# Kernel optimization log

Measured on AMD Instinct MI355X. Metric: run time of the kernel, lower is better.

The kernel has to match this reference:

```python
import jax, jax.numpy as jnp
import numpy as np

B, H, S, D = 2, 12, 2048, 64


def setup_inputs() -> dict:
    key = jax.random.key(0)
    kq, kk, kv = jax.random.split(key, 3)
    q = jax.random.normal(kq, (B, H, S, D), dtype=jnp.float32)
    k = jax.random.normal(kk, (B, H, S, D), dtype=jnp.float32)
    v = jax.random.normal(kv, (B, H, S, D), dtype=jnp.float32)
    # causal mask: True = attend (keep), lower triangle
    mask = jnp.tril(jnp.ones((S, S), dtype=bool))
    return {"q": q, "k": k, "v": v, "mask": mask}


def reference(q, k, v, mask):
    dim = q.shape[-1]
    # [B,H,S,S] scores
    scores = jnp.einsum("bhqd,bhkd->bhqk", q, k) / jnp.sqrt(jnp.asarray(dim, q.dtype))
    # dynamic mask-direction logic from the original module:
    # if the mask is denser in the strict upper triangle, True means "mask out";
    # otherwise True means "keep".
    sq = mask.shape[-1]
    sample = mask.reshape(-1, sq, sq)[0]
    upper = jnp.triu(jnp.ones_like(sample, dtype=bool), k=1)
    flip = jnp.sum(sample & upper) > jnp.sum(sample & ~upper)
    keep = jnp.where(flip, ~mask, mask)  # True = keep
    neg_inf = jnp.asarray(-jnp.inf, scores.dtype)
    scores = jnp.where(keep, scores, neg_inf)
    weights = jax.nn.softmax(scores, axis=-1)
    # dropout with p_drop=0.0 is the identity
    return jnp.einsum("bhqk,bhkd->bhqd", weights, v)
```

## Files before the change

kernel.cpp:

```cpp
#include <hip/hip_runtime.h>
#include <hip/hip_bf16.h>


#define SEQ 2048
#define DH 64
#define NHEADS 24
#define BN 64
#define LDK 72
#define ELEMS_PER_TENSOR (NHEADS * SEQ * DH)
#define NSLOT5 (NHEADS * 16 * 4)
#define WS_BF16  ((size_t)3 * ELEMS_PER_TENSOR * 2)
#define WS_FA7   (WS_BF16 + (size_t)NSLOT5 * 8192 * 2 + (size_t)NSLOT5 * 128 * 4)

typedef float f32x4 __attribute__((ext_vector_type(4)));
typedef __bf16 bf16x8 __attribute__((ext_vector_type(8)));
typedef __bf16 bf16x4 __attribute__((ext_vector_type(4)));

#if __has_builtin(__builtin_amdgcn_exp2f)
#define EXP2F(x) __builtin_amdgcn_exp2f(x)
#else
#define EXP2F(x) exp2f(x)
#endif

#define QSCALE 0.1803368801111204f

__global__ __launch_bounds__(256)
void prep_kernel(const float* __restrict__ q, const float* __restrict__ k,
                 const float* __restrict__ v,
                 __bf16* __restrict__ qs, __bf16* __restrict__ ks,
                 __bf16* __restrict__ vt)
{
    __shared__ __bf16 T[64][LDK];
    const int bx = blockIdx.x;
    const int tid = threadIdx.x;
    if (bx < 3072) {
        const int t = bx * 256 + tid;
        const int half = ELEMS_PER_TENSOR / 8;
        const bool is_q = t < half;
        const int idx = (is_q ? t : t - half) * 8;
        const float* src = is_q ? q : k;
        const float sc = is_q ? QSCALE : 1.0f;
        f32x4 a = *(const f32x4*)(src + idx);
        f32x4 b = *(const f32x4*)(src + idx + 4);
        bf16x8 o;
        #pragma unroll
        for (int j = 0; j < 4; ++j) { o[j] = (__bf16)(a[j] * sc); o[4 + j] = (__bf16)(b[j] * sc); }
        *(bf16x8*)((is_q ? qs : ks) + idx) = o;
    } else {
        const int b2 = bx - 3072;
        const int bh = b2 >> 5;
        const int s0 = (b2 & 31) * 64;
        const int r = tid >> 2, c0 = (tid & 3) * 16;
        const float* vp = v + (size_t)bh * SEQ * DH + (size_t)(s0 + r) * DH + c0;
        __bf16 tmp[16];
        #pragma unroll
        for (int jj = 0; jj < 16; ++jj) tmp[jj] = (__bf16)vp[jj];
        *(bf16x8*)&T[r][c0]     = *(bf16x8*)&tmp[0];
        *(bf16x8*)&T[r][c0 + 8] = *(bf16x8*)&tmp[8];
        __syncthreads();
        const int d = tid >> 2, j0 = (tid & 3) * 16;
        __bf16 o[16];
        #pragma unroll
        for (int jj = 0; jj < 16; ++jj) o[jj] = T[j0 + jj][d];
        __bf16* op = vt + (size_t)bh * DH * SEQ + (size_t)d * SEQ + s0 + j0;
        *(bf16x8*)op       = *(bf16x8*)&o[0];
        *(bf16x8*)(op + 8) = *(bf16x8*)&o[8];
    }
}

__global__ __launch_bounds__(256, 3)
void fa7_kernel(const __bf16* __restrict__ qs, const __bf16* __restrict__ ks,
                const __bf16* __restrict__ vt,
                __bf16* __restrict__ opart, float* __restrict__ lpart)
{
    const int bx = blockIdx.x;
    const int xcd = bx & 7;
    const int sub = bx >> 3;
    const int bh = (sub / 40) * 8 + xcd;
    const int rem = 39 - (sub % 40);
    int mt2, st;
    if      (rem >= 36) { mt2 = 15; st = 36; }
    else if (rem >= 32) { mt2 = 14; st = 32; }
    else if (rem >= 28) { mt2 = 13; st = 28; }
    else if (rem >= 24) { mt2 = 12; st = 24; }
    else if (rem >= 21) { mt2 = 11; st = 21; }
    else if (rem >= 18) { mt2 = 10; st = 18; }
    else if (rem >= 15) { mt2 = 9;  st = 15; }
    else if (rem >= 12) { mt2 = 8;  st = 12; }
    else if (rem >= 10) { mt2 = 7;  st = 10; }
    else if (rem >= 8)  { mt2 = 6;  st = 8; }
    else if (rem >= 6)  { mt2 = 5;  st = 6; }
    else if (rem >= 4)  { mt2 = 4;  st = 4; }
    else                { mt2 = rem; st = rem; }
    const int chunk = rem - st;
    const int jt0 = chunk * 8;
    const int jt_end = min(jt0 + 8, 2 * mt2 + 2);
    const int q0 = mt2 * 128;

    const int tid = threadIdx.x;
    const int w = tid >> 6, lane = tid & 63;
    const int g = lane >> 4, li = lane & 15;

    __shared__ __bf16 Ks[2][64 * 64];
    __shared__ __bf16 Vs[2][64 * 64];
    __shared__ __bf16 Ps[4 * 32 * 64];

    const __bf16* qh = qs + (size_t)bh * SEQ * DH;
    const __bf16* kh = ks + (size_t)bh * SEQ * DH;
    const __bf16* vh = vt + (size_t)bh * DH * SEQ;

    bf16x8 qf[2][2];
    #pragma unroll
    for (int a = 0; a < 2; ++a) {
        const __bf16* qp = qh + (size_t)(q0 + w * 32 + a * 16 + li) * DH + g * 8;
        qf[a][0] = *(const bf16x8*)qp;
        qf[a][1] = *(const bf16x8*)(qp + 32);
    }

    bf16x8 ones;
    #pragma unroll
    for (int j = 0; j < 8; ++j) ones[j] = (__bf16)1.0f;

    f32x4 acc[2][4] = {};
    f32x4 accl[2] = {};

    const int srow0 = tid >> 3;
    const int sg    = tid & 7;

    bf16x8 kr[2], vr[2];
    #pragma unroll
    for (int s = 0; s < 2; ++s) {
        const int row = s * 32 + srow0;
        const int lg = sg ^ (row & 7);
        kr[s] = *(const bf16x8*)(kh + (size_t)(jt0 * BN + row) * DH + lg * 8);
        vr[s] = *(const bf16x8*)(vh + (size_t)row * SEQ + jt0 * BN + lg * 8);
    }
    #pragma unroll
    for (int s = 0; s < 2; ++s) {
        *(bf16x8*)((char*)Ks[0] + s * 4096 + tid * 16) = kr[s];
        *(bf16x8*)((char*)Vs[0] + s * 4096 + tid * 16) = vr[s];
    }
    if (jt0 + 1 < jt_end) {
        const int kv1 = (jt0 + 1) * BN;
        #pragma unroll
        for (int s = 0; s < 2; ++s) {
            const int row = s * 32 + srow0;
            const int lg = sg ^ (row & 7);
            kr[s] = *(const bf16x8*)(kh + (size_t)(kv1 + row) * DH + lg * 8);
            vr[s] = *(const bf16x8*)(vh + (size_t)row * SEQ + kv1 + lg * 8);
        }
    }
    __syncthreads();

    int buf = 0;
    for (int jt = jt0; jt < jt_end; ++jt) {
        if (jt + 1 < jt_end) {
            #pragma unroll
            for (int s = 0; s < 2; ++s) {
                *(bf16x8*)((char*)Ks[buf ^ 1] + s * 4096 + tid * 16) = kr[s];
                *(bf16x8*)((char*)Vs[buf ^ 1] + s * 4096 + tid * 16) = vr[s];
            }
        }
        if (jt + 2 < jt_end) {
            const int kv2 = (jt + 2) * BN;
            #pragma unroll
            for (int s = 0; s < 2; ++s) {
                const int row = s * 32 + srow0;
                const int lg = sg ^ (row & 7);
                kr[s] = *(const bf16x8*)(kh + (size_t)(kv2 + row) * DH + lg * 8);
                vr[s] = *(const bf16x8*)(vh + (size_t)row * SEQ + kv2 + lg * 8);
            }
        }

        const char* Kb = (const char*)Ks[buf];
        const char* Vb = (const char*)Vs[buf];
        float s4[2][4][4];
        #pragma unroll
        for (int t = 0; t < 4; ++t) {
            f32x4 sa0 = {}, sa1 = {};
            #pragma unroll
            for (int c = 0; c < 2; ++c) {
                bf16x8 kf = *(const bf16x8*)(Kb +
                    (t * 16 + li) * 128 + (((c * 4 + g) ^ (li & 7)) << 4));
                sa0 = __builtin_amdgcn_mfma_f32_16x16x32_bf16(kf, qf[0][c], sa0, 0, 0, 0);
                sa1 = __builtin_amdgcn_mfma_f32_16x16x32_bf16(kf, qf[1][c], sa1, 0, 0, 0);
            }
            #pragma unroll
            for (int r = 0; r < 4; ++r) { s4[0][t][r] = sa0[r]; s4[1][t][r] = sa1[r]; }
        }

        if (jt >= 2 * mt2) {
            #pragma unroll
            for (int a = 0; a < 2; ++a) {
                const int qr = q0 + w * 32 + a * 16 + li;
                #pragma unroll
                for (int t = 0; t < 4; ++t) {
                    #pragma unroll
                    for (int r = 0; r < 4; ++r)
                        if (jt * 64 + t * 16 + g * 4 + r > qr) s4[a][t][r] = -1e30f;
                }
            }
        }

        #pragma unroll
        for (int a = 0; a < 2; ++a) {
            const int row = a * 16 + li;
            #pragma unroll
            for (int t = 0; t < 4; ++t) {
                bf16x4 p4;
                #pragma unroll
                for (int r = 0; r < 4; ++r) p4[r] = (__bf16)EXP2F(s4[a][t][r]);
                const int pg = (t * 2 + (g >> 1)) ^ (li & 7);
                *(bf16x4*)((char*)Ps + w * 4096 + row * 128 + (pg << 4) + ((g & 1) << 3)) = p4;
            }
        }

        #pragma unroll
        for (int c = 0; c < 2; ++c) {
            const int pgp = ((c * 4 + g) ^ (li & 7)) << 4;
            bf16x8 pf0 = *(const bf16x8*)((const char*)Ps + w * 4096 + li * 128 + pgp);
            bf16x8 pf1 = *(const bf16x8*)((const char*)Ps + w * 4096 + (16 + li) * 128 + pgp);
            accl[0] = __builtin_amdgcn_mfma_f32_16x16x32_bf16(pf0, ones, accl[0], 0, 0, 0);
            accl[1] = __builtin_amdgcn_mfma_f32_16x16x32_bf16(pf1, ones, accl[1], 0, 0, 0);
            #pragma unroll
            for (int t = 0; t < 4; ++t) {
                bf16x8 vf = *(const bf16x8*)(Vb + (t * 16 + li) * 128 + pgp);
                acc[0][t] = __builtin_amdgcn_mfma_f32_16x16x32_bf16(pf0, vf, acc[0][t], 0, 0, 0);
                acc[1][t] = __builtin_amdgcn_mfma_f32_16x16x32_bf16(pf1, vf, acc[1][t], 0, 0, 0);
            }
        }

        if (jt + 1 < jt_end) __syncthreads();
        buf ^= 1;
    }

    const int slot = (bh * 16 + mt2) * 4 + chunk;
    __bf16* po = opart + (size_t)slot * 8192;
    #pragma unroll
    for (int a = 0; a < 2; ++a) {
        #pragma unroll
        for (int r = 0; r < 4; ++r) {
            const int row = w * 32 + a * 16 + g * 4 + r;
            __bf16* op = po + row * 64 + li;
            #pragma unroll
            for (int t = 0; t < 4; ++t) op[t * 16] = (__bf16)acc[a][t][r];
            if (li == 0) lpart[(size_t)slot * 128 + row] = accl[a][r];
        }
    }
}

__global__ __launch_bounds__(256)
void fa_reduce(const __bf16* __restrict__ opart, const float* __restrict__ lpart,
               float* __restrict__ out)
{
    const int bx = blockIdx.x;
    const int bh = bx >> 4, mt2 = bx & 15;
    const int nc = (mt2 >> 2) + 1;
    const int base = (bh * 16 + mt2) * 4;
    const int tid = threadIdx.x;
    #pragma unroll
    for (int rnd = 0; rnd < 8; ++rnd) {
        const int flat = rnd * 1024 + tid * 4;
        const int row = flat >> 6;
        float o0 = 0, o1 = 0, o2 = 0, o3 = 0, l = 0;
        for (int c = 0; c < nc; ++c) {
            bf16x4 ov = *(const bf16x4*)(opart + (size_t)(base + c) * 8192 + flat);
            o0 += (float)ov[0]; o1 += (float)ov[1]; o2 += (float)ov[2]; o3 += (float)ov[3];
            l += lpart[(size_t)(base + c) * 128 + row];
        }
        const float inv = 1.0f / l;
        f32x4 res = { o0 * inv, o1 * inv, o2 * inv, o3 * inv };
        *(f32x4*)(out + (size_t)bh * SEQ * DH + (size_t)mt2 * 8192 + flat) = res;
    }
}

__global__ __launch_bounds__(256, 2)
void fa_causal_kernel(const float* __restrict__ q, const float* __restrict__ k,
                      const float* __restrict__ v, float* __restrict__ out)
{
    const int mt = 31 - (blockIdx.x & 31);
    const int bh = blockIdx.x >> 5;
    const int tid = threadIdx.x;
    const int w = tid >> 6, lane = tid & 63;
    const int g = lane >> 4, li = lane & 15;
    const int m0 = mt * 64;
    __shared__ __bf16 KsF[BN][LDK];
    __shared__ __bf16 VsF[DH][LDK];
    __shared__ __bf16 PsF[4][16][LDK];
    const size_t head_off = (size_t)bh * SEQ * DH;
    const float* qh = q + head_off;
    const float* kh = k + head_off;
    const float* vh = v + head_off;
    float* oh = out + head_off;
    const int qrow = m0 + w * 16 + li;
    bf16x8 qf[2];
    {
        const float* qp = qh + (size_t)qrow * DH + g * 8;
        #pragma unroll
        for (int c = 0; c < 2; ++c) {
            const float* p = qp + c * 32;
            #pragma unroll
            for (int jj = 0; jj < 8; ++jj) qf[c][jj] = (__bf16)p[jj];
        }
    }
    f32x4 acc[4] = {};
    float mrow[4], lrow[4];
    #pragma unroll
    for (int r = 0; r < 4; ++r) { mrow[r] = -1e30f; lrow[r] = 0.0f; }
    const float scale = 0.125f;
    const int srow = tid >> 2, scol = (tid & 3) * 16;
    for (int jt = 0; jt <= mt; ++jt) {
        const int kv0 = jt * BN;
        __syncthreads();
        {
            const float* kp = kh + (size_t)(kv0 + srow) * DH + scol;
            __bf16 tmp[16];
            #pragma unroll
            for (int jj = 0; jj < 16; ++jj) tmp[jj] = (__bf16)kp[jj];
            *(bf16x8*)&KsF[srow][scol]     = *(bf16x8*)&tmp[0];
            *(bf16x8*)&KsF[srow][scol + 8] = *(bf16x8*)&tmp[8];
            const float* vp = vh + (size_t)(kv0 + srow) * DH + scol;
            #pragma unroll
            for (int jj = 0; jj < 16; ++jj) VsF[scol + jj][srow] = (__bf16)vp[jj];
        }
        __syncthreads();
        float s4[4][4];
        #pragma unroll
        for (int t = 0; t < 4; ++t) {
            f32x4 sa = {};
            #pragma unroll
            for (int c = 0; c < 2; ++c) {
                bf16x8 kfr = *(const bf16x8*)&KsF[t * 16 + li][c * 32 + g * 8];
                sa = __builtin_amdgcn_mfma_f32_16x16x32_bf16(qf[c], kfr, sa, 0, 0, 0);
            }
            #pragma unroll
            for (int r = 0; r < 4; ++r) s4[t][r] = sa[r] * scale;
        }
        if (jt == mt) {
            #pragma unroll
            for (int t = 0; t < 4; ++t) {
                const int col = kv0 + t * 16 + li;
                #pragma unroll
                for (int r = 0; r < 4; ++r)
                    if (col > m0 + w * 16 + g * 4 + r) s4[t][r] = -1e30f;
            }
        }
        #pragma unroll
        for (int r = 0; r < 4; ++r) {
            float mx = fmaxf(fmaxf(s4[0][r], s4[1][r]), fmaxf(s4[2][r], s4[3][r]));
            #pragma unroll
            for (int off = 1; off < 16; off <<= 1)
                mx = fmaxf(mx, __shfl_xor(mx, off, 64));
            const float mnew = fmaxf(mrow[r], mx);
            const float alpha = __expf(mrow[r] - mnew);
            mrow[r] = mnew;
            float ps = 0.0f;
            #pragma unroll
            for (int t = 0; t < 4; ++t) {
                const float p = __expf(s4[t][r] - mnew);
                s4[t][r] = p;
                ps += p;
            }
            #pragma unroll
            for (int off = 1; off < 16; off <<= 1)
                ps += __shfl_xor(ps, off, 64);
            lrow[r] = lrow[r] * alpha + ps;
            #pragma unroll
            for (int t = 0; t < 4; ++t) acc[t][r] *= alpha;
        }
        #pragma unroll
        for (int t = 0; t < 4; ++t)
            #pragma unroll
            for (int r = 0; r < 4; ++r)
                PsF[w][g * 4 + r][t * 16 + li] = (__bf16)s4[t][r];
        __syncthreads();
        #pragma unroll
        for (int c = 0; c < 2; ++c) {
            bf16x8 pf = *(const bf16x8*)&PsF[w][li][c * 32 + g * 8];
            #pragma unroll
            for (int t = 0; t < 4; ++t) {
                bf16x8 vfr = *(const bf16x8*)&VsF[t * 16 + li][c * 32 + g * 8];
                acc[t] = __builtin_amdgcn_mfma_f32_16x16x32_bf16(pf, vfr, acc[t], 0, 0, 0);
            }
        }
    }
    #pragma unroll
    for (int r = 0; r < 4; ++r) {
        const int row = m0 + w * 16 + g * 4 + r;
        const float inv = 1.0f / lrow[r];
        float* op = oh + (size_t)row * DH + li;
        #pragma unroll
        for (int t = 0; t < 4; ++t) op[t * 16] = acc[t][r] * inv;
    }
}

extern "C" void kernel_launch(void* const* d_in, const int* in_sizes, int n_in,
                              void* d_out, int out_size, void* d_ws, size_t ws_size,
                              hipStream_t stream) {
    (void)in_sizes; (void)n_in; (void)out_size;
    const float* q = (const float*)d_in[0];
    const float* k = (const float*)d_in[1];
    const float* v = (const float*)d_in[2];
    float* out = (float*)d_out;

    if (ws_size >= WS_FA7) {
        __bf16* qs = (__bf16*)d_ws;
        __bf16* ks = qs + ELEMS_PER_TENSOR;
        __bf16* vt = ks + ELEMS_PER_TENSOR;
        __bf16* opart = (__bf16*)((char*)d_ws + WS_BF16);
        float* lpart = (float*)((char*)d_ws + WS_BF16 + (size_t)NSLOT5 * 8192 * 2);
        prep_kernel<<<dim3(3072 + 768), dim3(256), 0, stream>>>(q, k, v, qs, ks, vt);
        fa7_kernel<<<dim3(NHEADS * 40), dim3(256), 0, stream>>>(qs, ks, vt, opart, lpart);
        fa_reduce<<<dim3(NHEADS * 16), dim3(256), 0, stream>>>(opart, lpart, out);
    } else {
        fa_causal_kernel<<<dim3(NHEADS * 32), dim3(256), 0, stream>>>(q, k, v, out);
    }
}
```

Measured before the change: 133.5 us.

## Feed P to PV MFMA directly from registers via 16x16x16 bf16 instruction

Removes the shared-memory round trip for the softmax probabilities. The exp'd score fragments now go straight into the A operand of 16x16x16 bf16 MFMAs, whose input layout matches the score accumulator layout. The Ps LDS buffer is dropped and launch bounds are raised to allow four blocks per CU. The cost is twice as many MFMA instructions, each with half the K depth, plus narrower V fragment loads from LDS.

```diff
diff --git a/kernel.cpp b/kernel.cpp
--- a/kernel.cpp
+++ b/kernel.cpp
@@ -15,6 +15,7 @@
 typedef float f32x4 __attribute__((ext_vector_type(4)));
 typedef __bf16 bf16x8 __attribute__((ext_vector_type(8)));
 typedef __bf16 bf16x4 __attribute__((ext_vector_type(4)));
+typedef short short4v __attribute__((ext_vector_type(4)));
 
 #if __has_builtin(__builtin_amdgcn_exp2f)
 #define EXP2F(x) __builtin_amdgcn_exp2f(x)
@@ -23,6 +24,19 @@
 #endif
 
 #define QSCALE 0.1803368801111204f
+
+static __device__ __forceinline__ f32x4 mfma16_bf16(bf16x4 a, bf16x4 b, f32x4 c)
+{
+#if defined(__HIP_DEVICE_COMPILE__)
+    short4v as, bs;
+    __builtin_memcpy(&as, &a, 8);
+    __builtin_memcpy(&bs, &b, 8);
+    return __builtin_amdgcn_mfma_f32_16x16x16bf16_1k(as, bs, c, 0, 0, 0);
+#else
+    (void)a; (void)b;
+    return c;
+#endif
+}
 
 __global__ __launch_bounds__(256)
 void prep_kernel(const float* __restrict__ q, const float* __restrict__ k,
@@ -68,8 +82,8 @@
     }
 }
 
-__global__ __launch_bounds__(256, 3)
-void fa7_kernel(const __bf16* __restrict__ qs, const __bf16* __restrict__ ks,
+__global__ __launch_bounds__(256, 4)
+void fa8_kernel(const __bf16* __restrict__ qs, const __bf16* __restrict__ ks,
                 const __bf16* __restrict__ vt,
                 __bf16* __restrict__ opart, float* __restrict__ lpart)
 {
@@ -103,7 +117,6 @@
 
     __shared__ __bf16 Ks[2][64 * 64];
     __shared__ __bf16 Vs[2][64 * 64];
-    __shared__ __bf16 Ps[4 * 32 * 64];
 
     const __bf16* qh = qs + (size_t)bh * SEQ * DH;
     const __bf16* kh = ks + (size_t)bh * SEQ * DH;
@@ -117,9 +130,9 @@
         qf[a][1] = *(const bf16x8*)(qp + 32);
     }
 
-    bf16x8 ones;
-    #pragma unroll
-    for (int j = 0; j < 8; ++j) ones[j] = (__bf16)1.0f;
+    bf16x4 ones4;
+    #pragma unroll
+    for (int j = 0; j < 4; ++j) ones4[j] = (__bf16)1.0f;
 
     f32x4 acc[2][4] = {};
     f32x4 accl[2] = {};
@@ -202,31 +215,25 @@
             }
         }
 
-        #pragma unroll
-        for (int a = 0; a < 2; ++a) {
-            const int row = a * 16 + li;
-            #pragma unroll
-            for (int t = 0; t < 4; ++t) {
-                bf16x4 p4;
+        bf16x4 pf[2][4];
+        #pragma unroll
+        for (int a = 0; a < 2; ++a)
+            #pragma unroll
+            for (int t = 0; t < 4; ++t)
                 #pragma unroll
-                for (int r = 0; r < 4; ++r) p4[r] = (__bf16)EXP2F(s4[a][t][r]);
-                const int pg = (t * 2 + (g >> 1)) ^ (li & 7);
-                *(bf16x4*)((char*)Ps + w * 4096 + row * 128 + (pg << 4) + ((g & 1) << 3)) = p4;
-            }
-        }
-
-        #pragma unroll
-        for (int c = 0; c < 2; ++c) {
-            const int pgp = ((c * 4 + g) ^ (li & 7)) << 4;
-            bf16x8 pf0 = *(const bf16x8*)((const char*)Ps + w * 4096 + li * 128 + pgp);
-            bf16x8 pf1 = *(const bf16x8*)((const char*)Ps + w * 4096 + (16 + li) * 128 + pgp);
-            accl[0] = __builtin_amdgcn_mfma_f32_16x16x32_bf16(pf0, ones, accl[0], 0, 0, 0);
-            accl[1] = __builtin_amdgcn_mfma_f32_16x16x32_bf16(pf1, ones, accl[1], 0, 0, 0);
-            #pragma unroll
-            for (int t = 0; t < 4; ++t) {
-                bf16x8 vf = *(const bf16x8*)(Vb + (t * 16 + li) * 128 + pgp);
-                acc[0][t] = __builtin_amdgcn_mfma_f32_16x16x32_bf16(pf0, vf, acc[0][t], 0, 0, 0);
-                acc[1][t] = __builtin_amdgcn_mfma_f32_16x16x32_bf16(pf1, vf, acc[1][t], 0, 0, 0);
+                for (int r = 0; r < 4; ++r)
+                    pf[a][t][r] = (__bf16)EXP2F(s4[a][t][r]);
+
+        #pragma unroll
+        for (int t = 0; t < 4; ++t) {
+            accl[0] = mfma16_bf16(pf[0][t], ones4, accl[0]);
+            accl[1] = mfma16_bf16(pf[1][t], ones4, accl[1]);
+            #pragma unroll
+            for (int nt = 0; nt < 4; ++nt) {
+                bf16x4 vf = *(const bf16x4*)(Vb + (nt * 16 + li) * 128 +
+                    (((2 * t + (g >> 1)) ^ (li & 7)) << 4) + ((g & 1) << 3));
+                acc[0][nt] = mfma16_bf16(pf[0][t], vf, acc[0][nt]);
+                acc[1][nt] = mfma16_bf16(pf[1][t], vf, acc[1][nt]);
             }
         }
 
@@ -410,7 +417,7 @@
         __bf16* opart = (__bf16*)((char*)d_ws + WS_BF16);
         float* lpart = (float*)((char*)d_ws + WS_BF16 + (size_t)NSLOT5 * 8192 * 2);
         prep_kernel<<<dim3(3072 + 768), dim3(256), 0, stream>>>(q, k, v, qs, ks, vt);
-        fa7_kernel<<<dim3(NHEADS * 40), dim3(256), 0, stream>>>(qs, ks, vt, opart, lpart);
+        fa8_kernel<<<dim3(NHEADS * 40), dim3(256), 0, stream>>>(qs, ks, vt, opart, lpart);
         fa_reduce<<<dim3(NHEADS * 16), dim3(256), 0, stream>>>(opart, lpart, out);
     } else {
         fa_causal_kernel<<<dim3(NHEADS * 32), dim3(256), 0, stream>>>(q, k, v, out);
```

Result: slower. 147.5 us (+10.4%).

## Split KV range into finer chunks and fuse Q conversion into attention kernel

Applied to the files above, without the earlier changes.

The causal attention kernel now splits each 128-row query tile's key range into chunks of 4 key tiles instead of 8, raising the grid from 960 to 1728 blocks for finer load balance. The slot count and reduce kernel are adjusted to match. Q is no longer pre-converted to bf16 in the prep kernel; each attention block reads fp32 Q directly and scales and converts it in registers. This removes a prep pass and workspace traffic for Q, at the cost of more partial outputs to write and reduce and more redundant Q loads across chunks.

```diff
diff --git a/kernel.cpp b/kernel.cpp
--- a/kernel.cpp
+++ b/kernel.cpp
@@ -8,9 +8,9 @@
 #define BN 64
 #define LDK 72
 #define ELEMS_PER_TENSOR (NHEADS * SEQ * DH)
-#define NSLOT5 (NHEADS * 16 * 4)
-#define WS_BF16  ((size_t)3 * ELEMS_PER_TENSOR * 2)
-#define WS_FA7   (WS_BF16 + (size_t)NSLOT5 * 8192 * 2 + (size_t)NSLOT5 * 128 * 4)
+#define NSLOT10 (NHEADS * 16 * 8)
+#define WS_KV    ((size_t)2 * ELEMS_PER_TENSOR * 2)
+#define WS_FA10  (WS_KV + (size_t)NSLOT10 * 8192 * 2 + (size_t)NSLOT10 * 128 * 4)
 
 typedef float f32x4 __attribute__((ext_vector_type(4)));
 typedef __bf16 bf16x8 __attribute__((ext_vector_type(8)));
@@ -25,29 +25,22 @@
 #define QSCALE 0.1803368801111204f
 
 __global__ __launch_bounds__(256)
-void prep_kernel(const float* __restrict__ q, const float* __restrict__ k,
-                 const float* __restrict__ v,
-                 __bf16* __restrict__ qs, __bf16* __restrict__ ks,
-                 __bf16* __restrict__ vt)
+void prep_kernel(const float* __restrict__ k, const float* __restrict__ v,
+                 __bf16* __restrict__ ks, __bf16* __restrict__ vt)
 {
     __shared__ __bf16 T[64][LDK];
     const int bx = blockIdx.x;
     const int tid = threadIdx.x;
-    if (bx < 3072) {
-        const int t = bx * 256 + tid;
-        const int half = ELEMS_PER_TENSOR / 8;
-        const bool is_q = t < half;
-        const int idx = (is_q ? t : t - half) * 8;
-        const float* src = is_q ? q : k;
-        const float sc = is_q ? QSCALE : 1.0f;
-        f32x4 a = *(const f32x4*)(src + idx);
-        f32x4 b = *(const f32x4*)(src + idx + 4);
+    if (bx < 1536) {
+        const int idx = (bx * 256 + tid) * 8;
+        f32x4 a = *(const f32x4*)(k + idx);
+        f32x4 b = *(const f32x4*)(k + idx + 4);
         bf16x8 o;
         #pragma unroll
-        for (int j = 0; j < 4; ++j) { o[j] = (__bf16)(a[j] * sc); o[4 + j] = (__bf16)(b[j] * sc); }
-        *(bf16x8*)((is_q ? qs : ks) + idx) = o;
+        for (int j = 0; j < 4; ++j) { o[j] = (__bf16)a[j]; o[4 + j] = (__bf16)b[j]; }
+        *(bf16x8*)(ks + idx) = o;
     } else {
-        const int b2 = bx - 3072;
+        const int b2 = bx - 1536;
         const int bh = b2 >> 5;
         const int s0 = (b2 & 31) * 64;
         const int r = tid >> 2, c0 = (tid & 3) * 16;
@@ -69,32 +62,34 @@
 }
 
 __global__ __launch_bounds__(256, 3)
-void fa7_kernel(const __bf16* __restrict__ qs, const __bf16* __restrict__ ks,
-                const __bf16* __restrict__ vt,
-                __bf16* __restrict__ opart, float* __restrict__ lpart)
+void fa10_kernel(const float* __restrict__ q, const __bf16* __restrict__ ks,
+                 const __bf16* __restrict__ vt,
+                 __bf16* __restrict__ opart, float* __restrict__ lpart)
 {
     const int bx = blockIdx.x;
     const int xcd = bx & 7;
     const int sub = bx >> 3;
-    const int bh = (sub / 40) * 8 + xcd;
-    const int rem = 39 - (sub % 40);
-    int mt2, st;
-    if      (rem >= 36) { mt2 = 15; st = 36; }
-    else if (rem >= 32) { mt2 = 14; st = 32; }
-    else if (rem >= 28) { mt2 = 13; st = 28; }
-    else if (rem >= 24) { mt2 = 12; st = 24; }
-    else if (rem >= 21) { mt2 = 11; st = 21; }
-    else if (rem >= 18) { mt2 = 10; st = 18; }
-    else if (rem >= 15) { mt2 = 9;  st = 15; }
-    else if (rem >= 12) { mt2 = 8;  st = 12; }
-    else if (rem >= 10) { mt2 = 7;  st = 10; }
-    else if (rem >= 8)  { mt2 = 6;  st = 8; }
-    else if (rem >= 6)  { mt2 = 5;  st = 6; }
-    else if (rem >= 4)  { mt2 = 4;  st = 4; }
-    else                { mt2 = rem; st = rem; }
-    const int chunk = rem - st;
-    const int jt0 = chunk * 8;
-    const int jt_end = min(jt0 + 8, 2 * mt2 + 2);
+    const int bh = (sub / 72) * 8 + xcd;
+    const int i = sub % 72;
+    int mt2, ch;
+    if      (i < 8)  { mt2 = 15; ch = i; }
+    else if (i < 16) { mt2 = 14; ch = i - 8; }
+    else if (i < 23) { mt2 = 13; ch = i - 16; }
+    else if (i < 30) { mt2 = 12; ch = i - 23; }
+    else if (i < 36) { mt2 = 11; ch = i - 30; }
+    else if (i < 42) { mt2 = 10; ch = i - 36; }
+    else if (i < 47) { mt2 = 9;  ch = i - 42; }
+    else if (i < 52) { mt2 = 8;  ch = i - 47; }
+    else if (i < 56) { mt2 = 7;  ch = i - 52; }
+    else if (i < 60) { mt2 = 6;  ch = i - 56; }
+    else if (i < 63) { mt2 = 5;  ch = i - 60; }
+    else if (i < 66) { mt2 = 4;  ch = i - 63; }
+    else if (i < 68) { mt2 = 3;  ch = i - 66; }
+    else if (i < 70) { mt2 = 2;  ch = i - 68; }
+    else if (i < 71) { mt2 = 1;  ch = 0; }
+    else             { mt2 = 0;  ch = 0; }
+    const int jt0 = ch * 4;
+    const int jt_end = min(jt0 + 4, 2 * mt2 + 2);
     const int q0 = mt2 * 128;
 
     const int tid = threadIdx.x;
@@ -105,16 +100,24 @@
     __shared__ __bf16 Vs[2][64 * 64];
     __shared__ __bf16 Ps[4 * 32 * 64];
 
-    const __bf16* qh = qs + (size_t)bh * SEQ * DH;
     const __bf16* kh = ks + (size_t)bh * SEQ * DH;
     const __bf16* vh = vt + (size_t)bh * DH * SEQ;
 
     bf16x8 qf[2][2];
     #pragma unroll
     for (int a = 0; a < 2; ++a) {
-        const __bf16* qp = qh + (size_t)(q0 + w * 32 + a * 16 + li) * DH + g * 8;
-        qf[a][0] = *(const bf16x8*)qp;
-        qf[a][1] = *(const bf16x8*)(qp + 32);
+        const float* qp = q + (size_t)bh * SEQ * DH +
+                          (size_t)(q0 + w * 32 + a * 16 + li) * DH + g * 8;
+        #pragma unroll
+        for (int c = 0; c < 2; ++c) {
+            f32x4 x0 = *(const f32x4*)(qp + c * 32);
+            f32x4 x1 = *(const f32x4*)(qp + c * 32 + 4);
+            #pragma unroll
+            for (int j = 0; j < 4; ++j) {
+                qf[a][c][j]     = (__bf16)(x0[j] * QSCALE);
+                qf[a][c][4 + j] = (__bf16)(x1[j] * QSCALE);
+            }
+        }
     }
 
     bf16x8 ones;
@@ -234,7 +237,7 @@
         buf ^= 1;
     }
 
-    const int slot = (bh * 16 + mt2) * 4 + chunk;
+    const int slot = (bh * 16 + mt2) * 8 + ch;
     __bf16* po = opart + (size_t)slot * 8192;
     #pragma unroll
     for (int a = 0; a < 2; ++a) {
@@ -255,8 +258,8 @@
 {
     const int bx = blockIdx.x;
     const int bh = bx >> 4, mt2 = bx & 15;
-    const int nc = (mt2 >> 2) + 1;
-    const int base = (bh * 16 + mt2) * 4;
+    const int nc = (mt2 + 2) >> 1;
+    const int base = (bh * 16 + mt2) * 8;
     const int tid = threadIdx.x;
     #pragma unroll
     for (int rnd = 0; rnd < 8; ++rnd) {
@@ -403,14 +406,13 @@
     const float* v = (const float*)d_in[2];
     float* out = (float*)d_out;
 
-    if (ws_size >= WS_FA7) {
-        __bf16* qs = (__bf16*)d_ws;
-        __bf16* ks = qs + ELEMS_PER_TENSOR;
+    if (ws_size >= WS_FA10) {
+        __bf16* ks = (__bf16*)d_ws;
         __bf16* vt = ks + ELEMS_PER_TENSOR;
-        __bf16* opart = (__bf16*)((char*)d_ws + WS_BF16);
-        float* lpart = (float*)((char*)d_ws + WS_BF16 + (size_t)NSLOT5 * 8192 * 2);
-        prep_kernel<<<dim3(3072 + 768), dim3(256), 0, stream>>>(q, k, v, qs, ks, vt);
-        fa7_kernel<<<dim3(NHEADS * 40), dim3(256), 0, stream>>>(qs, ks, vt, opart, lpart);
+        __bf16* opart = (__bf16*)((char*)d_ws + WS_KV);
+        float* lpart = (float*)((char*)d_ws + WS_KV + (size_t)NSLOT10 * 8192 * 2);
+        prep_kernel<<<dim3(1536 + 768), dim3(256), 0, stream>>>(k, v, ks, vt);
+        fa10_kernel<<<dim3(1728), dim3(256), 0, stream>>>(q, ks, vt, opart, lpart);
         fa_reduce<<<dim3(NHEADS * 16), dim3(256), 0, stream>>>(opart, lpart, out);
     } else {
         fa_causal_kernel<<<dim3(NHEADS * 32), dim3(256), 0, stream>>>(q, k, v, out);
```

Measured after the change: 139.0 us. +4.1%, slower.
